# Optimization experiments

Hardware: AMD Instinct MI355X
Metric: run time of the kernel (lower is better)

The kernel has to match this reference:

```python
import jax, jax.numpy as jnp
import numpy as np

NUM_CAPS = 10       # J: output capsules
PREV_NODES = 16384  # P: input capsules (16*32*32)
IN_CH = 8           # D: input capsule dim
OUT_CH = 16         # O: output capsule dim
BATCH = 32
ROUTING_ITERS = 3


def squash(s):
    # s: (..., O). v = (|s|^2 / (1+|s|^2)) * s / |s|
    sq = jnp.sum(s * s, axis=-1, keepdims=True)
    return s * (sq / ((1.0 + sq) * jnp.sqrt(sq)))


def setup_inputs() -> dict:
    key = jax.random.key(0)
    kx, kw = jax.random.split(key)
    x = jax.random.normal(kx, (BATCH, PREV_NODES, IN_CH), dtype=jnp.float32)
    W = jax.random.normal(kw, (NUM_CAPS, PREV_NODES, IN_CH, OUT_CH), dtype=jnp.float32)
    return {"x": x, "W": W}


def reference(x, W):
    # u_hat[b,j,p,:] = x[b,p,:] @ W[j,p,:,:]  -> (B, J, P, O)
    u_hat = jnp.einsum('bpd,jpdo->bjpo', x, W)
    temp_u_hat = jax.lax.stop_gradient(u_hat)
    B = x.shape[0]
    b = jnp.zeros((B, NUM_CAPS, PREV_NODES, 1), dtype=u_hat.dtype)
    for _ in range(ROUTING_ITERS - 1):
        c = jax.nn.softmax(b, axis=1)                   # over output capsules
        s = jnp.sum(c * temp_u_hat, axis=2)             # (B, J, O)
        v = squash(s)
        uv = jnp.einsum('bjpo,bjo->bjp', temp_u_hat, v)[..., None]
        b = b + uv
    c = jax.nn.softmax(b, axis=1)
    s = jnp.sum(c * u_hat, axis=2)
    v = squash(s)                                       # (B, J, O)
    return v
```

## Files before the change

kernel.cpp:

```cpp
#include <hip/hip_runtime.h>

typedef _Float16 half_t;
typedef half_t h2 __attribute__((ext_vector_type(2)));
typedef half_t h4 __attribute__((ext_vector_type(4)));
typedef float f4 __attribute__((ext_vector_type(4)));

#define J 10
#define P 16384
#define D 8
#define O 16
#define B 32

#define PTILE 16
#define NB (P / PTILE)
#define SJO (B * J * O)

#define WT_PLS 2576
#define WT_PLH (WT_PLS / 2)
#define XS_OFF (PTILE * WT_PLS)
#define VL_OFF (XS_OFF + PTILE * B * 16)
#define VL_STRIDE 84
#define SMEM_BYTES (VL_OFF + B * VL_STRIDE * 4)

template <int CTRL>
__device__ __forceinline__ float dpp_mov_f(float v) {
    return __int_as_float(__builtin_amdgcn_update_dpp(
        0, __float_as_int(v), CTRL, 0xF, 0xF, true));
}
__device__ __forceinline__ float row_sum16(float v) {
    v += dpp_mov_f<0xB1>(v);
    v += dpp_mov_f<0x4E>(v);
    v += dpp_mov_f<0x124>(v);
    v += dpp_mov_f<0x128>(v);
    return v;
}

__device__ __forceinline__ h2 pkrtz(float a, float b) {
    return __builtin_bit_cast(h2, __builtin_amdgcn_cvt_pkrtz(a, b));
}

__device__ __forceinline__ float xadd16(float v) {
#if __has_builtin(__builtin_amdgcn_permlane16_swap)
    auto r = __builtin_amdgcn_permlane16_swap(__float_as_uint(v),
                                              __float_as_uint(v), false, false);
    return __uint_as_float(r[0]) + __uint_as_float(r[1]);
#else
    return v + __shfl_xor(v, 16, 64);
#endif
}
__device__ __forceinline__ float xadd32(float v) {
#if __has_builtin(__builtin_amdgcn_permlane32_swap)
    auto r = __builtin_amdgcn_permlane32_swap(__float_as_uint(v),
                                              __float_as_uint(v), false, false);
    return __uint_as_float(r[0]) + __uint_as_float(r[1]);
#else
    return v + __shfl_xor(v, 32, 64);
#endif
}

union U4H { uint4 u; h2 h[4]; };
union U2H { uint2 u2; h2 h[2]; h4 v; };
union U1H { unsigned u; h2 h; };

__global__ __launch_bounds__(512, 4) void caps_pass(
    const float* __restrict__ x, const float* __restrict__ W,
    const unsigned* __restrict__ vh, float* __restrict__ s_acc, int first)
{
    __shared__ char smem[SMEM_BYTES];
    half_t* Wt = (half_t*)smem;
    half_t* xs = (half_t*)(smem + XS_OFF);
    unsigned* vls = (unsigned*)(smem + VL_OFF);
    float* s_blk = (float*)smem;

    const int tid = threadIdx.x;
    const int p0 = blockIdx.x * PTILE;

    {
        const int o4 = tid & 3, d = (tid >> 2) & 7, pl = tid >> 5;
        const float* src = W + (size_t)p0 * (D * O) + (size_t)tid * 4;
        half_t* dst = Wt + pl * WT_PLH + (o4 * 4) * 8 + d;
#pragma unroll
        for (int j = 0; j < J; ++j) {
            float4 f = *(const float4*)(src + (size_t)j * P * (D * O));
            half_t* dj = dst + j * 128;
            dj[0]  = (half_t)f.x;
            dj[8]  = (half_t)f.y;
            dj[16] = (half_t)f.z;
            dj[24] = (half_t)f.w;
        }
    }
    {
        const int bl = tid >> 4, pl = tid & 15;
        const float4* xp = (const float4*)(x + ((size_t)bl * P + p0 + pl) * D);
        float4 a = xp[0], c = xp[1];
        U4H pk;
        pk.h[0] = pkrtz(a.x, a.y);
        pk.h[1] = pkrtz(a.z, a.w);
        pk.h[2] = pkrtz(c.x, c.y);
        pk.h[3] = pkrtz(c.z, c.w);
        *(uint4*)(xs + (size_t)(pl * 32 + bl) * 8) = pk.u;
    }
    if (!first && tid < B * J) {
        const int b = tid / J, j = tid - b * J;
        const uint4* s = (const uint4*)(vh + (size_t)tid * 8);
        uint4* dvl = (uint4*)(vls + b * VL_STRIDE + j * 8);
        dvl[0] = s[0];
        dvl[1] = s[1];
    }

    const int lane = tid & 63;
    const int wv   = tid >> 6;
    const int bh   = wv >> 2;
    const int wid2 = wv & 3;
    const int bl16 = lane & 15;
    const int q    = lane >> 4;
    const unsigned kmask = (q < 2) ? 0xFFFFFFFFu : 0u;
    const int vbase = (bh * 16 + bl16) * VL_STRIDE + q * 2;

    __syncthreads();

    f4 acc[J];
#pragma unroll
    for (int j = 0; j < J; ++j) acc[j] = (f4){0.f, 0.f, 0.f, 0.f};
    const f4 zf = (f4){0.f, 0.f, 0.f, 0.f};

#pragma unroll 1
    for (int pi = 0; pi < 4; ++pi) {
        const int pl = wid2 * 4 + pi;

        U2H xv;
        xv.u2 = *(const uint2*)(xs + (size_t)(pl * 32 + bh * 16 + bl16) * 8
                                + 4 * (q & 1));
        xv.u2.x &= kmask;
        xv.u2.y &= kmask;
        const h4 bfrag = xv.v;

        const half_t* wbase = Wt + pl * WT_PLH + bl16 * 8 + 4 * (q & 1);

        h2 uh[J][2];
        float lg[J];
#pragma unroll
        for (int j = 0; j < J; ++j) {
            const h4 af = *(const h4*)(wbase + j * 128);
            f4 u = __builtin_amdgcn_mfma_f32_16x16x16f16(af, bfrag, zf, 0, 0, 0);
            if (first) {
#pragma unroll
                for (int r = 0; r < 4; ++r)
                    acc[j][r] = fmaf(0.1f, u[r], acc[j][r]);
            } else {
                uh[j][0] = pkrtz(u[0], u[1]);
                uh[j][1] = pkrtz(u[2], u[3]);
                U2H vf;
                vf.u2 = *(const uint2*)(vls + vbase + j * 8);
                lg[j] = __builtin_amdgcn_fdot2(uh[j][1], vf.h[1],
                        __builtin_amdgcn_fdot2(uh[j][0], vf.h[0], 0.f, false),
                        false);
            }
        }

        if (!first) {
#pragma unroll
            for (int j = 0; j < J; ++j) lg[j] = xadd16(lg[j]);
#pragma unroll
            for (int j = 0; j < J; ++j) lg[j] = xadd32(lg[j]);
            float e[J], Z = 0.f;
#pragma unroll
            for (int j = 0; j < J; ++j) { e[j] = __expf(lg[j]); Z += e[j]; }
            const float rZ = __builtin_amdgcn_rcpf(Z);
#pragma unroll
            for (int j = 0; j < J; ++j) {
                const float c = e[j] * rZ;
                acc[j][0] = fmaf(c, (float)uh[j][0][0], acc[j][0]);
                acc[j][1] = fmaf(c, (float)uh[j][0][1], acc[j][1]);
                acc[j][2] = fmaf(c, (float)uh[j][1][0], acc[j][2]);
                acc[j][3] = fmaf(c, (float)uh[j][1][1], acc[j][3]);
            }
        }
    }

    __syncthreads();
#pragma unroll 1
    for (int r = 0; r < 2; ++r) {
        if (bh == r) {
#pragma unroll
            for (int j = 0; j < J; ++j)
                *(f4*)&s_blk[(size_t)(wid2 * 16 + bl16) * 164 + j * 16 + 4 * q]
                    = acc[j];
        }
        __syncthreads();
        for (int t = tid; t < 16 * 160; t += 512) {
            const int bl = t / 160, rr = t - bl * 160;
            const float v = s_blk[bl * 164 + rr] + s_blk[(16 + bl) * 164 + rr]
                          + s_blk[(32 + bl) * 164 + rr] + s_blk[(48 + bl) * 164 + rr];
            atomicAdd(&s_acc[(size_t)(r * 16 + bl) * 160 + rr], v);
        }
        __syncthreads();
    }
}

__global__ __launch_bounds__(256) void caps_squash(
    float* __restrict__ s_acc, float* __restrict__ Vsum,
    unsigned* __restrict__ vh, float* __restrict__ out, int write_out)
{
    const int b = blockIdx.x;
    const int o = threadIdx.x & 15;
    const int j = threadIdx.x >> 4;
    const bool act = j < J;
    const int idx = (b * J + (act ? j : 0)) * O + o;
    float s = act ? s_acc[idx] : 0.f;
    const float sq = row_sum16(s * s);
    float vnew = 0.f;
    if (act) {
        const float scale = sqrtf(sq) / (1.f + sq);
        const float v = s * scale;
        vnew = Vsum[idx] + v;
        Vsum[idx] = vnew;
        s_acc[idx] = 0.f;
        if (write_out) out[idx] = v;
    }
    const float vpart = __shfl_xor(vnew, 1, 64);
    if (act && !(o & 1)) {
        U1H t; t.h = pkrtz(vnew, vpart);
        vh[(size_t)(b * J + j) * 8 + (o >> 1)] = t.u;
    }
}

__global__ __launch_bounds__(256) void caps_zero(float* __restrict__ ws)
{
    const int i = blockIdx.x * 256 + threadIdx.x;
    if (i < 2 * SJO) ws[i] = 0.f;
}

extern "C" void kernel_launch(void* const* d_in, const int* in_sizes, int n_in,
                              void* d_out, int out_size, void* d_ws, size_t ws_size,
                              hipStream_t stream)
{
    const float* x = (const float*)d_in[0];
    const float* W = (const float*)d_in[1];
    float* out = (float*)d_out;

    float* s_acc = (float*)d_ws;
    float* Vsum  = s_acc + SJO;
    unsigned* vh = (unsigned*)(Vsum + SJO);

    caps_zero<<<dim3(40), 256, 0, stream>>>(s_acc);

    for (int it = 0; it < 3; ++it) {
        caps_pass<<<dim3(NB), 512, 0, stream>>>(x, W, vh, s_acc, it == 0 ? 1 : 0);
        caps_squash<<<dim3(B), 256, 0, stream>>>(s_acc, Vsum, vh, out, it == 2 ? 1 : 0);
    }
}
```

Before: 250.5 us.

## Double-buffer W and x tiles across four sub-tiles per block

Each block now processes four 8-node tiles instead of one 16-node tile. The next tile's W and x are prefetched into registers while the current tile is computed from shared memory, then written into a second LDS buffer. This hides global-load latency and divides the atomic reduction of partial s by about half, since there are fewer blocks. In exchange there are fewer blocks (512), each with more LDS and more registers, so occupancy and parallelism may drop.

```diff
diff --git a/kernel.cpp b/kernel.cpp
--- a/kernel.cpp
+++ b/kernel.cpp
@@ -11,14 +11,17 @@
 #define O 16
 #define B 32
 
-#define PTILE 16
-#define NB (P / PTILE)
+#define PTILE 8
+#define TILES_PER_BLK 4
+#define NBLK (P / PTILE / TILES_PER_BLK)
 #define SJO (B * J * O)
 
 #define WT_PLS 2576
 #define WT_PLH (WT_PLS / 2)
-#define XS_OFF (PTILE * WT_PLS)
-#define VL_OFF (XS_OFF + PTILE * B * 16)
+#define WT_BYTES (PTILE * WT_PLS)
+#define XS_BYTES (PTILE * B * 16)
+#define BUF_BYTES (WT_BYTES + XS_BYTES)
+#define VL_OFF (2 * BUF_BYTES)
 #define VL_STRIDE 84
 #define SMEM_BYTES (VL_OFF + B * VL_STRIDE * 4)
 
@@ -67,45 +70,65 @@
     const unsigned* __restrict__ vh, float* __restrict__ s_acc, int first)
 {
     __shared__ char smem[SMEM_BYTES];
-    half_t* Wt = (half_t*)smem;
-    half_t* xs = (half_t*)(smem + XS_OFF);
     unsigned* vls = (unsigned*)(smem + VL_OFF);
     float* s_blk = (float*)smem;
 
     const int tid = threadIdx.x;
-    const int p0 = blockIdx.x * PTILE;
-
-    {
-        const int o4 = tid & 3, d = (tid >> 2) & 7, pl = tid >> 5;
-        const float* src = W + (size_t)p0 * (D * O) + (size_t)tid * 4;
-        half_t* dst = Wt + pl * WT_PLH + (o4 * 4) * 8 + d;
-#pragma unroll
-        for (int j = 0; j < J; ++j) {
-            float4 f = *(const float4*)(src + (size_t)j * P * (D * O));
-            half_t* dj = dst + j * 128;
-            dj[0]  = (half_t)f.x;
-            dj[8]  = (half_t)f.y;
-            dj[16] = (half_t)f.z;
-            dj[24] = (half_t)f.w;
-        }
-    }
-    {
-        const int bl = tid >> 4, pl = tid & 15;
-        const float4* xp = (const float4*)(x + ((size_t)bl * P + p0 + pl) * D);
-        float4 a = xp[0], c = xp[1];
-        U4H pk;
-        pk.h[0] = pkrtz(a.x, a.y);
-        pk.h[1] = pkrtz(a.z, a.w);
-        pk.h[2] = pkrtz(c.x, c.y);
-        pk.h[3] = pkrtz(c.z, c.w);
-        *(uint4*)(xs + (size_t)(pl * 32 + bl) * 8) = pk.u;
-    }
+    const int tile0 = blockIdx.x * TILES_PER_BLK;
+
+    const int w_o4 = tid & 3, w_d = (tid >> 2) & 7, w_pl = (tid >> 5) & 7;
+    const int w_jh = tid >> 8;
+    const int x_pl = tid & 7, x_bl = (tid >> 3) & 31, x_hf = tid >> 8;
+
     if (!first && tid < B * J) {
         const int b = tid / J, j = tid - b * J;
         const uint4* s = (const uint4*)(vh + (size_t)tid * 8);
         uint4* dvl = (uint4*)(vls + b * VL_STRIDE + j * 8);
         dvl[0] = s[0];
         dvl[1] = s[1];
+    }
+
+    float4 wf0, wf1, wf2, wf3, wf4;
+    float4 xf;
+
+#define LOADT(t)                                                               \
+    {                                                                          \
+        const int p0 = (tile0 + (t)) * PTILE;                                  \
+        const float* wsrc = W + (size_t)(p0 + w_pl) * 128 + w_d * 16 + w_o4 * 4; \
+        const size_t jstep = (size_t)P * 128;                                  \
+        const float* wj = wsrc + (size_t)(w_jh * 5) * jstep;                   \
+        wf0 = *(const float4*)(wj);                                            \
+        wf1 = *(const float4*)(wj + jstep);                                    \
+        wf2 = *(const float4*)(wj + 2 * jstep);                                \
+        wf3 = *(const float4*)(wj + 3 * jstep);                                \
+        wf4 = *(const float4*)(wj + 4 * jstep);                                \
+        xf = *(const float4*)(x + ((size_t)x_bl * P + p0 + x_pl) * D + x_hf * 4); \
+    }
+
+#define WRITET(k)                                                              \
+    {                                                                          \
+        half_t* Wtw = (half_t*)(smem + (k) * BUF_BYTES);                       \
+        half_t* xsw = (half_t*)(smem + (k) * BUF_BYTES + WT_BYTES);            \
+        half_t* dst = Wtw + w_pl * WT_PLH + (w_o4 * 4) * 8 + w_d;              \
+        half_t* dj = dst + (w_jh * 5) * 128;                                   \
+        dj[0] = (half_t)wf0.x; dj[8] = (half_t)wf0.y;                          \
+        dj[16] = (half_t)wf0.z; dj[24] = (half_t)wf0.w;                        \
+        dj += 128;                                                             \
+        dj[0] = (half_t)wf1.x; dj[8] = (half_t)wf1.y;                          \
+        dj[16] = (half_t)wf1.z; dj[24] = (half_t)wf1.w;                        \
+        dj += 128;                                                             \
+        dj[0] = (half_t)wf2.x; dj[8] = (half_t)wf2.y;                          \
+        dj[16] = (half_t)wf2.z; dj[24] = (half_t)wf2.w;                        \
+        dj += 128;                                                             \
+        dj[0] = (half_t)wf3.x; dj[8] = (half_t)wf3.y;                          \
+        dj[16] = (half_t)wf3.z; dj[24] = (half_t)wf3.w;                        \
+        dj += 128;                                                             \
+        dj[0] = (half_t)wf4.x; dj[8] = (half_t)wf4.y;                          \
+        dj[16] = (half_t)wf4.z; dj[24] = (half_t)wf4.w;                        \
+        U2H pk;                                                                \
+        pk.h[0] = pkrtz(xf.x, xf.y);                                           \
+        pk.h[1] = pkrtz(xf.z, xf.w);                                           \
+        *(uint2*)(xsw + ((size_t)x_pl * 32 + x_bl) * 8 + x_hf * 4) = pk.u2;    \
     }
 
     const int lane = tid & 63;
@@ -117,68 +140,81 @@
     const unsigned kmask = (q < 2) ? 0xFFFFFFFFu : 0u;
     const int vbase = (bh * 16 + bl16) * VL_STRIDE + q * 2;
 
-    __syncthreads();
-
     f4 acc[J];
 #pragma unroll
     for (int j = 0; j < J; ++j) acc[j] = (f4){0.f, 0.f, 0.f, 0.f};
     const f4 zf = (f4){0.f, 0.f, 0.f, 0.f};
 
+    LOADT(0);
+    WRITET(0);
+    __syncthreads();
+
 #pragma unroll 1
-    for (int pi = 0; pi < 4; ++pi) {
-        const int pl = wid2 * 4 + pi;
-
-        U2H xv;
-        xv.u2 = *(const uint2*)(xs + (size_t)(pl * 32 + bh * 16 + bl16) * 8
-                                + 4 * (q & 1));
-        xv.u2.x &= kmask;
-        xv.u2.y &= kmask;
-        const h4 bfrag = xv.v;
-
-        const half_t* wbase = Wt + pl * WT_PLH + bl16 * 8 + 4 * (q & 1);
-
-        h2 uh[J][2];
-        float lg[J];
-#pragma unroll
-        for (int j = 0; j < J; ++j) {
-            const h4 af = *(const h4*)(wbase + j * 128);
-            f4 u = __builtin_amdgcn_mfma_f32_16x16x16f16(af, bfrag, zf, 0, 0, 0);
-            if (first) {
-#pragma unroll
-                for (int r = 0; r < 4; ++r)
-                    acc[j][r] = fmaf(0.1f, u[r], acc[j][r]);
-            } else {
-                uh[j][0] = pkrtz(u[0], u[1]);
-                uh[j][1] = pkrtz(u[2], u[3]);
-                U2H vf;
-                vf.u2 = *(const uint2*)(vls + vbase + j * 8);
-                lg[j] = __builtin_amdgcn_fdot2(uh[j][1], vf.h[1],
-                        __builtin_amdgcn_fdot2(uh[j][0], vf.h[0], 0.f, false),
-                        false);
+    for (int t = 0; t < TILES_PER_BLK; ++t) {
+        const int cur = t & 1;
+        if (t + 1 < TILES_PER_BLK) LOADT(t + 1);
+
+        const half_t* Wt = (const half_t*)(smem + cur * BUF_BYTES);
+        const half_t* xs = (const half_t*)(smem + cur * BUF_BYTES + WT_BYTES);
+
+#pragma unroll 1
+        for (int pi = 0; pi < 2; ++pi) {
+            const int pl = wid2 * 2 + pi;
+
+            U2H xv;
+            xv.u2 = *(const uint2*)(xs + (size_t)(pl * 32 + bh * 16 + bl16) * 8
+                                    + 4 * (q & 1));
+            xv.u2.x &= kmask;
+            xv.u2.y &= kmask;
+            const h4 bfrag = xv.v;
+
+            const half_t* wbase = Wt + pl * WT_PLH + bl16 * 8 + 4 * (q & 1);
+
+            h2 uh[J][2];
+            float lg[J];
+#pragma unroll
+            for (int j = 0; j < J; ++j) {
+                const h4 af = *(const h4*)(wbase + j * 128);
+                f4 u = __builtin_amdgcn_mfma_f32_16x16x16f16(af, bfrag, zf, 0, 0, 0);
+                if (first) {
+#pragma unroll
+                    for (int r = 0; r < 4; ++r)
+                        acc[j][r] = fmaf(0.1f, u[r], acc[j][r]);
+                } else {
+                    uh[j][0] = pkrtz(u[0], u[1]);
+                    uh[j][1] = pkrtz(u[2], u[3]);
+                    U2H vf;
+                    vf.u2 = *(const uint2*)(vls + vbase + j * 8);
+                    lg[j] = __builtin_amdgcn_fdot2(uh[j][1], vf.h[1],
+                            __builtin_amdgcn_fdot2(uh[j][0], vf.h[0], 0.f, false),
+                            false);
+                }
+            }
+
+            if (!first) {
+#pragma unroll
+                for (int j = 0; j < J; ++j) lg[j] = xadd16(lg[j]);
+#pragma unroll
+                for (int j = 0; j < J; ++j) lg[j] = xadd32(lg[j]);
+                float e[J], Z = 0.f;
+#pragma unroll
+                for (int j = 0; j < J; ++j) { e[j] = __expf(lg[j]); Z += e[j]; }
+                const float rZ = __builtin_amdgcn_rcpf(Z);
+#pragma unroll
+                for (int j = 0; j < J; ++j) {
+                    const float c = e[j] * rZ;
+                    acc[j][0] = fmaf(c, (float)uh[j][0][0], acc[j][0]);
+                    acc[j][1] = fmaf(c, (float)uh[j][0][1], acc[j][1]);
+                    acc[j][2] = fmaf(c, (float)uh[j][1][0], acc[j][2]);
+                    acc[j][3] = fmaf(c, (float)uh[j][1][1], acc[j][3]);
+                }
             }
         }
 
-        if (!first) {
-#pragma unroll
-            for (int j = 0; j < J; ++j) lg[j] = xadd16(lg[j]);
-#pragma unroll
-            for (int j = 0; j < J; ++j) lg[j] = xadd32(lg[j]);
-            float e[J], Z = 0.f;
-#pragma unroll
-            for (int j = 0; j < J; ++j) { e[j] = __expf(lg[j]); Z += e[j]; }
-            const float rZ = __builtin_amdgcn_rcpf(Z);
-#pragma unroll
-            for (int j = 0; j < J; ++j) {
-                const float c = e[j] * rZ;
-                acc[j][0] = fmaf(c, (float)uh[j][0][0], acc[j][0]);
-                acc[j][1] = fmaf(c, (float)uh[j][0][1], acc[j][1]);
-                acc[j][2] = fmaf(c, (float)uh[j][1][0], acc[j][2]);
-                acc[j][3] = fmaf(c, (float)uh[j][1][1], acc[j][3]);
-            }
-        }
-    }
-
-    __syncthreads();
+        if (t + 1 < TILES_PER_BLK) WRITET(cur ^ 1);
+        __syncthreads();
+    }
+
 #pragma unroll 1
     for (int r = 0; r < 2; ++r) {
         if (bh == r) {
@@ -246,7 +282,7 @@
     caps_zero<<<dim3(40), 256, 0, stream>>>(s_acc);
 
     for (int it = 0; it < 3; ++it) {
-        caps_pass<<<dim3(NB), 512, 0, stream>>>(x, W, vh, s_acc, it == 0 ? 1 : 0);
+        caps_pass<<<dim3(NBLK), 512, 0, stream>>>(x, W, vh, s_acc, it == 0 ? 1 : 0);
         caps_squash<<<dim3(B), 256, 0, stream>>>(s_acc, Vsum, vh, out, it == 2 ? 1 : 0);
     }
 }
```

After: 271.8 us. 1.09x slower.
